# Performance work log

Measured on AMD Instinct MI355X. Metric: run time of the kernel, lower is better.

Reference implementation:

```python
import jax, jax.numpy as jnp
import numpy as np

H = 512        # hidden_dim
D_IN = 512     # input_dim
N_ACT = 16     # output_dim
DICT = 8192    # dict_len (episodic memory slots)
B = 4096       # batch
N_CYCLES = 10  # LCA iterations
DT_T = 0.6     # LCA dt/tau
EPS = 1e-8     # cosine-similarity eps


def setup_inputs() -> dict:
    key = jax.random.key(0)
    ks = jax.random.split(key, 12)
    NHT = 4 * H + 3  # (N_VSIG+1)*H + N_SSIG
    s = lambda i, shape, sc=1.0: jax.random.normal(ks[i], shape, jnp.float32) * sc
    return {
        "x_t": s(0, (1, B, D_IN)),
        "h_prev": s(1, (1, B, H), 0.1),
        "c_prev": s(2, (1, B, H), 0.1),
        "W_i2h": s(3, (NHT, D_IN), 1.0 / np.sqrt(D_IN)),
        "b_i2h": jnp.zeros((NHT,), jnp.float32),
        "W_h2h": s(4, (NHT, H), 1.0 / np.sqrt(H)),
        "b_h2h": jnp.zeros((NHT,), jnp.float32),
        "vals": s(5, (DICT, H), 0.1),  # episodic memory table
        "W_ih": s(6, (H, H), 1.0 / np.sqrt(H)),
        "b_ih": jnp.zeros((H,), jnp.float32),
        "W_actor": s(7, (N_ACT, H), 1.0 / np.sqrt(H)),
        "b_actor": jnp.zeros((N_ACT,), jnp.float32),
        "W_critic": s(8, (1, H), 1.0 / np.sqrt(H)),
        "b_critic": jnp.zeros((1,), jnp.float32),
        "mem_ptr": 0,
    }


def _lca(sim, leak, comp, w_input):
    # Leaky competing accumulator over memory slots; sim:[B,DICT], scalars:[B,1]
    ff = w_input * sim
    def step(V, _):
        inhib = comp * (jnp.sum(V, axis=-1, keepdims=True) - V)  # lateral inhibition (excl. self)
        V = jax.nn.relu(V + DT_T * (ff - leak * V - inhib))
        return V, None
    V, _ = jax.lax.scan(step, jnp.zeros_like(sim), None, length=N_CYCLES)
    return V


def reference(x_t, h_prev, c_prev, W_i2h, b_i2h, W_h2h, b_h2h, vals,
              W_ih, b_ih, W_actor, b_actor, W_critic, b_critic, mem_ptr):
    x, h, c = x_t[0], h_prev[0], c_prev[0]  # [B, dim]
    preact = x @ W_i2h.T + b_i2h + h @ W_h2h.T + b_h2h  # [B, 4H+3]
    gates = jax.nn.sigmoid(preact[:, :3 * H])
    f_t = gates[:, :H]
    o_t = gates[:, H:2 * H]
    i_t = gates[:, 2 * H:3 * H]
    inps = jax.nn.sigmoid(preact[:, 3 * H + 0])[:, None]  # input strength (gain=1)
    leak = jax.nn.sigmoid(preact[:, 3 * H + 1])[:, None]
    comp = jax.nn.sigmoid(preact[:, 3 * H + 2])[:, None]
    c_new = jnp.tanh(preact[:, 3 * H + 3:])
    c_t = c * f_t + i_t * c_new
    # --- recall: cosine similarity vs memory, then LCA competition ---
    qn = jnp.linalg.norm(c_t, axis=-1, keepdims=True)        # [B,1]
    mn = jnp.linalg.norm(vals, axis=-1, keepdims=True)       # [DICT,1]
    sim = (c_t @ vals.T) / jnp.maximum(qn * mn.T, EPS)       # [B,DICT]
    w = _lca(sim, leak, comp, inps)                          # [B,DICT]
    m_t = w @ vals                                           # [B,H]
    cm_t = c_t + m_t
    # --- encode: ring-buffer scatter write of cm_t into memory ---
    idx = (mem_ptr + jnp.arange(B)) % DICT
    new_vals = vals.at[idx].set(cm_t)
    h_t = o_t * jnp.tanh(cm_t)
    # --- A2C head ---
    a2c_h = jax.nn.relu(h_t @ W_ih.T + b_ih)
    pi = jax.nn.softmax(a2c_h @ W_actor.T + b_actor, axis=-1)
    value = a2c_h @ W_critic.T + b_critic
    return pi, value, h_t, cm_t, m_t, new_vals
```

## Files before the change

### kernel.cpp

```cpp
#include <hip/hip_runtime.h>
#include <hip/hip_fp16.h>
#include <math.h>

#define HH    512
#define DICT  8192
#define BATCH 4096
#define NCYC  10
#define DTT   0.6f

#define BM  128
#define BKT 64

using f16x8 = __attribute__((ext_vector_type(8))) _Float16;
using f32x4 = __attribute__((ext_vector_type(4))) float;

__device__ __forceinline__ float sigmoidf_(float x) { return 1.0f / (1.0f + __expf(-x)); }

__device__ __forceinline__ float waveReduceSum(float v) {
#pragma unroll
  for (int o = 1; o < 64; o <<= 1) v += __shfl_xor(v, o);
  return v;
}

__device__ __forceinline__ void gld16(const void* g, void* l) {
  __builtin_amdgcn_global_load_lds(
      (const __attribute__((address_space(1))) void*)g,
      (__attribute__((address_space(3))) void*)l, 16, 0, 0);
}

template<int ROWS>
__device__ __forceinline__ void stage_tile(const __half* gbase, int ld, char* lds, int tid) {
  constexpr int ISS = ROWS * 8 / 256;
#pragma unroll
  for (int i = 0; i < ISS; ++i) {
    int cidx = i * 256 + tid;
    int row  = cidx >> 3;
    int slot = cidx & 7;
    int k4   = slot ^ (row & 7);
    gld16(gbase + (size_t)row * ld + k4 * 8, lds + cidx * 16);
  }
}

__device__ __forceinline__ f16x8 frag_ld(const char* lds, int row, int kchunk) {
  int slot = kchunk ^ (row & 7);
  return *(const f16x8*)(lds + row * 128 + slot * 16);
}

template<int FN>
__device__ __forceinline__ void tile_mfma(const char* As, const char* Bs,
                                          int lane, int wr, int wc, f32x4 (&acc)[4][FN]) {
  const int g = lane >> 4, r = lane & 15;
#pragma unroll
  for (int ks = 0; ks < 2; ++ks) {
    f16x8 af[4], bfr[FN];
#pragma unroll
    for (int i = 0; i < 4; ++i)
      af[i] = frag_ld(As, wr * 64 + i * 16 + r, ks * 4 + g);
#pragma unroll
    for (int j = 0; j < FN; ++j)
      bfr[j] = frag_ld(Bs, wc * (FN * 16) + j * 16 + r, ks * 4 + g);
#pragma unroll
    for (int i = 0; i < 4; ++i)
#pragma unroll
      for (int j = 0; j < FN; ++j)
        acc[i][j] = __builtin_amdgcn_mfma_f32_16x16x32_f16(af[i], bfr[j], acc[i][j], 0, 0, 0);
  }
}

template<int BN, int FN>
__device__ __forceinline__ void gemm_seg(const __half* A, int lda, const __half* B, int ldb,
                                         int m0, int n0, int K, char* lds, int tid,
                                         f32x4 (&acc)[4][FN]) {
  constexpr int ABYTES = BM * BKT * 2;
  constexpr int BBYTES = BN * BKT * 2;
  const int lane = tid & 63, wid = tid >> 6;
  const int wr = wid >> 1, wc = wid & 1;
  const int nt = K / BKT;
  const __half* Ab = A + (size_t)m0 * lda;
  const __half* Bb = B + (size_t)n0 * ldb;
  stage_tile<BM>(Ab, lda, lds, tid);
  stage_tile<BN>(Bb, ldb, lds + ABYTES, tid);
  __syncthreads();
  int cur = 0;
  for (int t = 0; t < nt - 1; ++t) {
    char* nxt = lds + (cur ^ 1) * (ABYTES + BBYTES);
    stage_tile<BM>(Ab + (t + 1) * BKT, lda, nxt, tid);
    stage_tile<BN>(Bb + (t + 1) * BKT, ldb, nxt + ABYTES, tid);
    char* curb = lds + cur * (ABYTES + BBYTES);
    tile_mfma<FN>(curb, curb + ABYTES, lane, wr, wc, acc);
    __syncthreads();
    cur ^= 1;
  }
  char* curb = lds + cur * (ABYTES + BBYTES);
  tile_mfma<FN>(curb, curb + ABYTES, lane, wr, wc, acc);
  __syncthreads();
}

__device__ __forceinline__ void zero_acc4(f32x4 (&a)[4][4]) {
  f32x4 z = {0.f, 0.f, 0.f, 0.f};
#pragma unroll
  for (int i = 0; i < 4; ++i)
#pragma unroll
    for (int j = 0; j < 4; ++j) a[i][j] = z;
}
__device__ __forceinline__ void zero_acc2(f32x4 (&a)[4][2]) {
  f32x4 z = {0.f, 0.f, 0.f, 0.f};
#pragma unroll
  for (int i = 0; i < 4; ++i)
#pragma unroll
    for (int j = 0; j < 2; ++j) a[i][j] = z;
}

__global__ __launch_bounds__(256) void k_prep_cvt(
    const float* __restrict__ x, const float* __restrict__ h,
    const float* __restrict__ Wi, const float* __restrict__ Wh, const float* __restrict__ Wih,
    __half* __restrict__ x_h, __half* __restrict__ h_h,
    __half* __restrict__ Wip_h, __half* __restrict__ Whp_h, __half* __restrict__ Wih_h) {
  int gq = blockIdx.x * 256 + threadIdx.x;
  const float* src; __half* dst; int si, di;
  if (gq < 524288) {
    src = x; dst = x_h; si = di = gq * 4;
  } else if (gq < 1048576) {
    src = h; dst = h_h; si = di = (gq - 524288) * 4;
  } else if (gq < 1310720) {
    int iq = gq - 1048576;
    int jp = iq >> 7, k4 = (iq & 127) << 2;
    int U = jp >> 6, g = (jp >> 4) & 3, r = jp & 15;
    int u = U * 16 + r;
    int orig = g * 512 + u + (g == 3 ? 3 : 0);
    src = Wi; dst = Wip_h; si = orig * 512 + k4; di = jp * 512 + k4;
  } else if (gq < 1572864) {
    int iq = gq - 1310720;
    int jp = iq >> 7, k4 = (iq & 127) << 2;
    int U = jp >> 6, g = (jp >> 4) & 3, r = jp & 15;
    int u = U * 16 + r;
    int orig = g * 512 + u + (g == 3 ? 3 : 0);
    src = Wh; dst = Whp_h; si = orig * 512 + k4; di = jp * 512 + k4;
  } else if (gq < 1638400) {
    int iq = gq - 1572864;
    src = Wih; dst = Wih_h; si = di = iq * 4;
  } else return;
  float4 v = *(const float4*)(src + si);
  *(__half2*)(dst + di)     = __floats2half2_rn(v.x, v.y);
  *(__half2*)(dst + di + 2) = __floats2half2_rn(v.z, v.w);
}

__global__ __launch_bounds__(256) void k_prep_vals(
    const float* __restrict__ vals, float* __restrict__ nv,
    __half* __restrict__ vals_h, float* __restrict__ rmn) {
  const int row  = blockIdx.x * 4 + (threadIdx.x >> 6);
  const int lane = threadIdx.x & 63;
  const float* vr = vals + (size_t)row * HH + lane * 8;
  float4 a = *(const float4*)(vr);
  float4 b = *(const float4*)(vr + 4);
  float* nvp = nv + (size_t)row * HH + lane * 8;
  *(float4*)(nvp)     = a;
  *(float4*)(nvp + 4) = b;
  __half* vh = vals_h + (size_t)row * HH + lane * 8;
  *(__half2*)(vh)     = __floats2half2_rn(a.x, a.y);
  *(__half2*)(vh + 2) = __floats2half2_rn(a.z, a.w);
  *(__half2*)(vh + 4) = __floats2half2_rn(b.x, b.y);
  *(__half2*)(vh + 6) = __floats2half2_rn(b.z, b.w);
  float ss = a.x * a.x + a.y * a.y + a.z * a.z + a.w * a.w
           + b.x * b.x + b.y * b.y + b.z * b.z + b.w * b.w;
  ss = waveReduceSum(ss);
  if (lane == 0) rmn[row] = 1.f / fmaxf(sqrtf(ss), 1e-12f);
}

__global__ __launch_bounds__(256) void k_tr(const float* __restrict__ vals, __half* __restrict__ vT) {
  __shared__ float tile[32][33];
  int r0 = blockIdx.x * 32, c0 = blockIdx.y * 32;
  int tr = threadIdx.x >> 5, tc = threadIdx.x & 31;
#pragma unroll
  for (int p = 0; p < 4; ++p)
    tile[tr + p * 8][tc] = vals[(size_t)(r0 + tr + p * 8) * HH + c0 + tc];
  __syncthreads();
#pragma unroll
  for (int p = 0; p < 4; ++p)
    vT[(size_t)(c0 + tr + p * 8) * DICT + r0 + tc] = __float2half(tile[tc][tr + p * 8]);
}

__global__ __launch_bounds__(256) void k_preact(
    const __half* __restrict__ x_h, const __half* __restrict__ h_h,
    const __half* __restrict__ Wip, const __half* __restrict__ Whp,
    const float* __restrict__ bi, const float* __restrict__ bh,
    const float* __restrict__ c_prev,
    float* __restrict__ ct, float* __restrict__ ot, __half* __restrict__ ct_h) {
  __shared__ char smem[2 * (BM * BKT * 2 + 128 * BKT * 2)] __attribute__((aligned(16)));
  const int tid = threadIdx.x;
  const int m0 = blockIdx.y * 128, n0 = blockIdx.x * 128;
  f32x4 acc[4][4]; zero_acc4(acc);
  gemm_seg<128, 4>(x_h, HH, Wip, HH, m0, n0, HH, smem, tid, acc);
  gemm_seg<128, 4>(h_h, HH, Whp, HH, m0, n0, HH, smem, tid, acc);
  const int lane = tid & 63, wid = tid >> 6, wr = wid >> 1, wc = wid & 1;
  const int r = lane & 15;
  const int u = ((n0 >> 6) + wc) * 16 + r;
  float bsum[4];
#pragma unroll
  for (int g = 0; g < 4; ++g) {
    int orig = g * 512 + u + (g == 3 ? 3 : 0);
    bsum[g] = bi[orig] + bh[orig];
  }
#pragma unroll
  for (int fi = 0; fi < 4; ++fi)
#pragma unroll
    for (int q = 0; q < 4; ++q) {
      int m = m0 + wr * 64 + fi * 16 + (lane >> 4) * 4 + q;
      float f  = sigmoidf_(acc[fi][0][q] + bsum[0]);
      float o  = sigmoidf_(acc[fi][1][q] + bsum[1]);
      float ii = sigmoidf_(acc[fi][2][q] + bsum[2]);
      float cn = tanhf(acc[fi][3][q] + bsum[3]);
      size_t off = (size_t)m * HH + u;
      float cc = c_prev[off] * f + ii * cn;
      ct[off] = cc; ot[off] = o; ct_h[off] = __float2half(cc);
    }
}

__global__ __launch_bounds__(256) void k_scalars(
    const float* __restrict__ x, const float* __restrict__ h,
    const float* __restrict__ Wi, const float* __restrict__ Wh,
    const float* __restrict__ bi, const float* __restrict__ bh,
    const float* __restrict__ ct,
    float* __restrict__ inps, float* __restrict__ leak,
    float* __restrict__ comp, float* __restrict__ rqn) {
  const int b = blockIdx.x, wid = threadIdx.x >> 6, lane = threadIdx.x & 63;
  const int j = lane * 8;
  if (wid < 3) {
    const float* wi = Wi + (size_t)(1536 + wid) * HH + j;
    const float* wh = Wh + (size_t)(1536 + wid) * HH + j;
    const float* xr = x + (size_t)b * HH + j;
    const float* hr = h + (size_t)b * HH + j;
    float4 xa = *(const float4*)(xr), xb = *(const float4*)(xr + 4);
    float4 wa = *(const float4*)(wi), wb = *(const float4*)(wi + 4);
    float4 ha = *(const float4*)(hr), hb = *(const float4*)(hr + 4);
    float4 va = *(const float4*)(wh), vb = *(const float4*)(wh + 4);
    float s = xa.x * wa.x + xa.y * wa.y + xa.z * wa.z + xa.w * wa.w
            + xb.x * wb.x + xb.y * wb.y + xb.z * wb.z + xb.w * wb.w
            + ha.x * va.x + ha.y * va.y + ha.z * va.z + ha.w * va.w
            + hb.x * vb.x + hb.y * vb.y + hb.z * vb.z + hb.w * vb.w;
    s = waveReduceSum(s);
    if (lane == 0) {
      float v = sigmoidf_(s + bi[1536 + wid] + bh[1536 + wid]);
      if (wid == 0) inps[b] = v; else if (wid == 1) leak[b] = v; else comp[b] = v;
    }
  } else {
    const float* cr = ct + (size_t)b * HH + j;
    float4 a = *(const float4*)(cr), d = *(const float4*)(cr + 4);
    float ss = a.x * a.x + a.y * a.y + a.z * a.z + a.w * a.w
             + d.x * d.x + d.y * d.y + d.z * d.z + d.w * d.w;
    ss = waveReduceSum(ss);
    if (lane == 0) rqn[b] = 1.f / fmaxf(sqrtf(ss), 1e-12f);
  }
}

__global__ __launch_bounds__(256) void k_sim(
    const __half* __restrict__ ct_h, const __half* __restrict__ vals_h,
    const float* __restrict__ rqn, const float* __restrict__ rmn,
    __half* __restrict__ sim_h) {
  __shared__ char smem[2 * (BM * BKT * 2 + 128 * BKT * 2)] __attribute__((aligned(16)));
  const int tid = threadIdx.x;
  const int m0 = blockIdx.y * 128, n0 = blockIdx.x * 128;
  f32x4 acc[4][4]; zero_acc4(acc);
  gemm_seg<128, 4>(ct_h, HH, vals_h, HH, m0, n0, HH, smem, tid, acc);
  const int lane = tid & 63, wid = tid >> 6, wr = wid >> 1, wc = wid & 1;
#pragma unroll
  for (int fi = 0; fi < 4; ++fi)
#pragma unroll
    for (int fj = 0; fj < 4; ++fj)
#pragma unroll
      for (int q = 0; q < 4; ++q) {
        int m = m0 + wr * 64 + fi * 16 + (lane >> 4) * 4 + q;
        int n = n0 + wc * 64 + fj * 16 + (lane & 15);
        sim_h[(size_t)m * DICT + n] = __float2half(acc[fi][fj][q] * rqn[m] * rmn[n]);
      }
}

__global__ __launch_bounds__(256) void k_lca(
    const __half* __restrict__ sim_h, const float* __restrict__ inps,
    const float* __restrict__ leak, const float* __restrict__ comp,
    __half* __restrict__ w_h) {
  const int b = blockIdx.x, t = threadIdx.x;
  const __half* srow = sim_h + (size_t)b * DICT + t * 32;
  const float ffs = DTT * inps[b];
  const float a   = 1.0f - DTT * leak[b] + DTT * comp[b];
  const float cdt = DTT * comp[b];
  float ff[32], V[32];
#pragma unroll
  for (int i = 0; i < 4; ++i) {
    f16x8 v8 = *(const f16x8*)(srow + i * 8);
#pragma unroll
    for (int j = 0; j < 8; ++j) { ff[i * 8 + j] = ffs * (float)v8[j]; V[i * 8 + j] = 0.f; }
  }
  __shared__ float ps[4];
  for (int it = 0; it < NCYC; ++it) {
    float s = 0.f;
#pragma unroll
    for (int i = 0; i < 32; ++i) s += V[i];
    s = waveReduceSum(s);
    if ((t & 63) == 0) ps[t >> 6] = s;
    __syncthreads();
    float S = ps[0] + ps[1] + ps[2] + ps[3];
    __syncthreads();
    float sub = cdt * S;
#pragma unroll
    for (int i = 0; i < 32; ++i) V[i] = fmaxf(fmaf(a, V[i], ff[i] - sub), 0.f);
  }
  __half* wrow = w_h + (size_t)b * DICT + t * 32;
#pragma unroll
  for (int i = 0; i < 4; ++i) {
    f16x8 o8;
#pragma unroll
    for (int j = 0; j < 8; ++j) o8[j] = (_Float16)V[i * 8 + j];
    *(f16x8*)(wrow + i * 8) = o8;
  }
}

__global__ __launch_bounds__(256) void k_mt_p(
    const __half* __restrict__ w_h, const __half* __restrict__ vT_h,
    float* __restrict__ partial) {
  __shared__ char smem[2 * (BM * BKT * 2 + 64 * BKT * 2)] __attribute__((aligned(16)));
  const int tid = threadIdx.x, bid = blockIdx.x;
  const int xcd = bid & 7, idx = bid >> 3;
  const int n = idx & 7, q = idx >> 3;
  const int g = (q << 3) | xcd;
  const int m = g >> 2, s = g & 3;
  const int m0 = m * 128, n0 = n * 64;
  f32x4 acc[4][2]; zero_acc2(acc);
  gemm_seg<64, 2>(w_h + s * 2048, DICT, vT_h + s * 2048, DICT, m0, n0, 2048, smem, tid, acc);
  const int lane = tid & 63, wid = tid >> 6, wr = wid >> 1, wc = wid & 1;
  float* pbase = partial + (size_t)s * (BATCH * HH);
#pragma unroll
  for (int fi = 0; fi < 4; ++fi)
#pragma unroll
    for (int fj = 0; fj < 2; ++fj)
#pragma unroll
      for (int qq = 0; qq < 4; ++qq) {
        int mm = m0 + wr * 64 + fi * 16 + (lane >> 4) * 4 + qq;
        int nn = n0 + wc * 32 + fj * 16 + (lane & 15);
        pbase[(size_t)mm * HH + nn] = acc[fi][fj][qq];
      }
}

__global__ __launch_bounds__(256) void k_mt_red(
    const float* __restrict__ partial,
    const float* __restrict__ ct, const float* __restrict__ ot, const int* __restrict__ mptr,
    float* __restrict__ out_mt, float* __restrict__ out_cmt, float* __restrict__ out_ht,
    float* __restrict__ out_nv, __half* __restrict__ ht_h) {
  const int i4 = blockIdx.x * 256 + threadIdx.x;
  const size_t off = (size_t)i4 * 4;
  const int m = i4 >> 7;
  float4 p  = *(const float4*)(partial + off);
  float4 p1 = *(const float4*)(partial + 2097152 + off);
  float4 p2 = *(const float4*)(partial + 4194304 + off);
  float4 p3 = *(const float4*)(partial + 6291456 + off);
  p.x += p1.x + p2.x + p3.x;
  p.y += p1.y + p2.y + p3.y;
  p.z += p1.z + p2.z + p3.z;
  p.w += p1.w + p2.w + p3.w;
  float4 c4 = *(const float4*)(ct + off);
  float4 o4 = *(const float4*)(ot + off);
  float4 cm, hv;
  cm.x = c4.x + p.x; hv.x = o4.x * tanhf(cm.x);
  cm.y = c4.y + p.y; hv.y = o4.y * tanhf(cm.y);
  cm.z = c4.z + p.z; hv.z = o4.z * tanhf(cm.z);
  cm.w = c4.w + p.w; hv.w = o4.w * tanhf(cm.w);
  *(float4*)(out_mt + off)  = p;
  *(float4*)(out_cmt + off) = cm;
  *(float4*)(out_ht + off)  = hv;
  *(__half2*)(ht_h + off)     = __floats2half2_rn(hv.x, hv.y);
  *(__half2*)(ht_h + off + 2) = __floats2half2_rn(hv.z, hv.w);
  const int nvrow = (mptr[0] + m) & (DICT - 1);
  *(float4*)(out_nv + (size_t)nvrow * HH + (off & 511)) = cm;
}

__global__ __launch_bounds__(256) void k_a2c(
    const __half* __restrict__ ht_h, const __half* __restrict__ Wih_h,
    const float* __restrict__ bih, float* __restrict__ a2c) {
  __shared__ char smem[2 * (BM * BKT * 2 + 64 * BKT * 2)] __attribute__((aligned(16)));
  const int tid = threadIdx.x;
  const int bid = blockIdx.x;
  const int xn = (bid >> 3) & 7, ym = (bid & 7) | ((bid >> 6) << 3);
  const int m0 = ym * 128, n0 = xn * 64;
  f32x4 acc[4][2]; zero_acc2(acc);
  gemm_seg<64, 2>(ht_h, HH, Wih_h, HH, m0, n0, HH, smem, tid, acc);
  const int lane = tid & 63, wid = tid >> 6, wr = wid >> 1, wc = wid & 1;
#pragma unroll
  for (int fi = 0; fi < 4; ++fi)
#pragma unroll
    for (int fj = 0; fj < 2; ++fj)
#pragma unroll
      for (int q = 0; q < 4; ++q) {
        int m = m0 + wr * 64 + fi * 16 + (lane >> 4) * 4 + q;
        int n = n0 + wc * 32 + fj * 16 + (lane & 15);
        a2c[(size_t)m * HH + n] = fmaxf(acc[fi][fj][q] + bih[n], 0.f);
      }
}

__global__ __launch_bounds__(256) void k_actor(
    const float* __restrict__ a2c,
    const float* __restrict__ Wact, const float* __restrict__ bact,
    const float* __restrict__ Wcr, const float* __restrict__ bcr,
    float* __restrict__ out_pi, float* __restrict__ out_val) {
  const int b = blockIdx.x * 4 + (threadIdx.x >> 6);
  const int lane = threadIdx.x & 63;
  const float* hrow = a2c + (size_t)b * HH;
  float4 a0 = *(const float4*)(hrow + (lane << 3));
  float4 a1 = *(const float4*)(hrow + (lane << 3) + 4);
  float lg[17];
#pragma unroll
  for (int o = 0; o < 17; ++o) {
    const float* wr = (o < 16) ? (Wact + (size_t)o * HH) : Wcr;
    float4 w0 = *(const float4*)(wr + (lane << 3));
    float4 w1 = *(const float4*)(wr + (lane << 3) + 4);
    float s = a0.x * w0.x + a0.y * w0.y + a0.z * w0.z + a0.w * w0.w
            + a1.x * w1.x + a1.y * w1.y + a1.z * w1.z + a1.w * w1.w;
    lg[o] = waveReduceSum(s);
  }
#pragma unroll
  for (int o = 0; o < 16; ++o) lg[o] += bact[o];
  float mx = lg[0];
#pragma unroll
  for (int o = 1; o < 16; ++o) mx = fmaxf(mx, lg[o]);
  float e[16], sum = 0.f;
#pragma unroll
  for (int o = 0; o < 16; ++o) { e[o] = __expf(lg[o] - mx); sum += e[o]; }
  float rs = 1.f / sum;
  if (lane == 0) {
#pragma unroll
    for (int o = 0; o < 16; ++o) out_pi[(size_t)b * 16 + o] = e[o] * rs;
    out_val[b] = lg[16] + bcr[0];
  }
}

extern "C" void kernel_launch(void* const* d_in, const int* in_sizes, int n_in,
                              void* d_out, int out_size, void* d_ws, size_t ws_size,
                              hipStream_t stream) {
  const float* x    = (const float*)d_in[0];
  const float* h    = (const float*)d_in[1];
  const float* c    = (const float*)d_in[2];
  const float* Wi   = (const float*)d_in[3];
  const float* bi   = (const float*)d_in[4];
  const float* Wh   = (const float*)d_in[5];
  const float* bh   = (const float*)d_in[6];
  const float* vals = (const float*)d_in[7];
  const float* Wih  = (const float*)d_in[8];
  const float* bih  = (const float*)d_in[9];
  const float* Wact = (const float*)d_in[10];
  const float* bact = (const float*)d_in[11];
  const float* Wcr  = (const float*)d_in[12];
  const float* bcr  = (const float*)d_in[13];
  const int*   mptr = (const int*)d_in[14];

  float* F = (float*)d_ws;
  __half* w_h    = (__half*)F;
  __half* sim_h   = (__half*)(F + 16777216);
  float*  a2c     = F + 16777216;
  float*  partial = F + 33554432;
  float*  ct     = F + 50331648;
  float*  ot     = F + 52428800;
  __half* ct_h   = (__half*)(F + 54525952);
  __half* vals_h = (__half*)(F + 55574528);
  __half* vT_h   = (__half*)(F + 57671680);
  __half* x_h    = (__half*)(F + 59768832);
  __half* ht_h   = x_h;
  __half* h_h    = (__half*)(F + 60817408);
  __half* Wip_h  = (__half*)(F + 61865984);
  __half* Whp_h  = (__half*)(F + 62423040);
  __half* Wih_h  = (__half*)(F + 62980096);
  float*  inps   = F + 63111168;
  float*  leak   = inps + 4096;
  float*  comp   = leak + 4096;
  float*  rqn    = comp + 4096;
  float*  rmn    = rqn + 4096;

  float* out     = (float*)d_out;
  float* out_pi  = out;
  float* out_val = out + 65536;
  float* out_ht  = out + 69632;
  float* out_cmt = out_ht + 2097152;
  float* out_mt  = out_cmt + 2097152;
  float* out_nv  = out_mt + 2097152;

  dim3 b256(256);
  k_prep_cvt <<<6400, b256, 0, stream>>>(x, h, Wi, Wh, Wih, x_h, h_h, Wip_h, Whp_h, Wih_h);
  k_prep_vals<<<2048, b256, 0, stream>>>(vals, out_nv, vals_h, rmn);
  k_tr <<<dim3(256, 16), b256, 0, stream>>>(vals, vT_h);
  k_preact <<<dim3(16, 32), b256, 0, stream>>>(x_h, h_h, Wip_h, Whp_h, bi, bh, c,
                                               ct, ot, ct_h);
  k_scalars<<<BATCH, b256, 0, stream>>>(x, h, Wi, Wh, bi, bh, ct, inps, leak, comp, rqn);
  k_sim    <<<dim3(64, 32), b256, 0, stream>>>(ct_h, vals_h, rqn, rmn, sim_h);
  k_lca    <<<BATCH, b256, 0, stream>>>(sim_h, inps, leak, comp, w_h);
  k_mt_p   <<<1024, b256, 0, stream>>>(w_h, vT_h, partial);
  k_mt_red <<<2048, b256, 0, stream>>>(partial, ct, ot, mptr,
                                       out_mt, out_cmt, out_ht, out_nv, ht_h);
  k_a2c    <<<256, b256, 0, stream>>>(ht_h, Wih_h, bih, a2c);
  k_actor  <<<BATCH / 4, b256, 0, stream>>>(a2c, Wact, bact, Wcr, bcr, out_pi, out_val);
}
```

Measured before the change: 234.8 us.

## Single-buffer GEMM LDS staging and merge three prep kernels into one launch

The shared GEMM segment drops its LDS double buffering. Each K-tile is now staged, synced, computed and synced again, which halves shared memory per block and may allow more resident blocks. The three prep kernels (fp16 conversion, vals copy/norm, vals transpose) are merged into one launch dispatched by block index, removing two launches. The cost is that global loads no longer overlap MFMA work inside each block, and each K-tile gets an extra barrier.

```diff
diff --git a/kernel.cpp b/kernel.cpp
--- a/kernel.cpp
+++ b/kernel.cpp
@@ -72,28 +72,18 @@
                                          int m0, int n0, int K, char* lds, int tid,
                                          f32x4 (&acc)[4][FN]) {
   constexpr int ABYTES = BM * BKT * 2;
-  constexpr int BBYTES = BN * BKT * 2;
   const int lane = tid & 63, wid = tid >> 6;
   const int wr = wid >> 1, wc = wid & 1;
   const int nt = K / BKT;
   const __half* Ab = A + (size_t)m0 * lda;
   const __half* Bb = B + (size_t)n0 * ldb;
-  stage_tile<BM>(Ab, lda, lds, tid);
-  stage_tile<BN>(Bb, ldb, lds + ABYTES, tid);
-  __syncthreads();
-  int cur = 0;
-  for (int t = 0; t < nt - 1; ++t) {
-    char* nxt = lds + (cur ^ 1) * (ABYTES + BBYTES);
-    stage_tile<BM>(Ab + (t + 1) * BKT, lda, nxt, tid);
-    stage_tile<BN>(Bb + (t + 1) * BKT, ldb, nxt + ABYTES, tid);
-    char* curb = lds + cur * (ABYTES + BBYTES);
-    tile_mfma<FN>(curb, curb + ABYTES, lane, wr, wc, acc);
+  for (int t = 0; t < nt; ++t) {
+    stage_tile<BM>(Ab + t * BKT, lda, lds, tid);
+    stage_tile<BN>(Bb + t * BKT, ldb, lds + ABYTES, tid);
     __syncthreads();
-    cur ^= 1;
-  }
-  char* curb = lds + cur * (ABYTES + BBYTES);
-  tile_mfma<FN>(curb, curb + ABYTES, lane, wr, wc, acc);
-  __syncthreads();
+    tile_mfma<FN>(lds, lds + ABYTES, lane, wr, wc, acc);
+    __syncthreads();
+  }
 }
 
 __device__ __forceinline__ void zero_acc4(f32x4 (&a)[4][4]) {
@@ -111,73 +101,74 @@
     for (int j = 0; j < 2; ++j) a[i][j] = z;
 }
 
-__global__ __launch_bounds__(256) void k_prep_cvt(
+__global__ __launch_bounds__(256) void k_prep(
     const float* __restrict__ x, const float* __restrict__ h,
     const float* __restrict__ Wi, const float* __restrict__ Wh, const float* __restrict__ Wih,
+    const float* __restrict__ vals,
     __half* __restrict__ x_h, __half* __restrict__ h_h,
-    __half* __restrict__ Wip_h, __half* __restrict__ Whp_h, __half* __restrict__ Wih_h) {
-  int gq = blockIdx.x * 256 + threadIdx.x;
-  const float* src; __half* dst; int si, di;
-  if (gq < 524288) {
-    src = x; dst = x_h; si = di = gq * 4;
-  } else if (gq < 1048576) {
-    src = h; dst = h_h; si = di = (gq - 524288) * 4;
-  } else if (gq < 1310720) {
-    int iq = gq - 1048576;
-    int jp = iq >> 7, k4 = (iq & 127) << 2;
-    int U = jp >> 6, g = (jp >> 4) & 3, r = jp & 15;
-    int u = U * 16 + r;
-    int orig = g * 512 + u + (g == 3 ? 3 : 0);
-    src = Wi; dst = Wip_h; si = orig * 512 + k4; di = jp * 512 + k4;
-  } else if (gq < 1572864) {
-    int iq = gq - 1310720;
-    int jp = iq >> 7, k4 = (iq & 127) << 2;
-    int U = jp >> 6, g = (jp >> 4) & 3, r = jp & 15;
-    int u = U * 16 + r;
-    int orig = g * 512 + u + (g == 3 ? 3 : 0);
-    src = Wh; dst = Whp_h; si = orig * 512 + k4; di = jp * 512 + k4;
-  } else if (gq < 1638400) {
-    int iq = gq - 1572864;
-    src = Wih; dst = Wih_h; si = di = iq * 4;
-  } else return;
-  float4 v = *(const float4*)(src + si);
-  *(__half2*)(dst + di)     = __floats2half2_rn(v.x, v.y);
-  *(__half2*)(dst + di + 2) = __floats2half2_rn(v.z, v.w);
-}
-
-__global__ __launch_bounds__(256) void k_prep_vals(
-    const float* __restrict__ vals, float* __restrict__ nv,
-    __half* __restrict__ vals_h, float* __restrict__ rmn) {
-  const int row  = blockIdx.x * 4 + (threadIdx.x >> 6);
-  const int lane = threadIdx.x & 63;
-  const float* vr = vals + (size_t)row * HH + lane * 8;
-  float4 a = *(const float4*)(vr);
-  float4 b = *(const float4*)(vr + 4);
-  float* nvp = nv + (size_t)row * HH + lane * 8;
-  *(float4*)(nvp)     = a;
-  *(float4*)(nvp + 4) = b;
-  __half* vh = vals_h + (size_t)row * HH + lane * 8;
-  *(__half2*)(vh)     = __floats2half2_rn(a.x, a.y);
-  *(__half2*)(vh + 2) = __floats2half2_rn(a.z, a.w);
-  *(__half2*)(vh + 4) = __floats2half2_rn(b.x, b.y);
-  *(__half2*)(vh + 6) = __floats2half2_rn(b.z, b.w);
-  float ss = a.x * a.x + a.y * a.y + a.z * a.z + a.w * a.w
-           + b.x * b.x + b.y * b.y + b.z * b.z + b.w * b.w;
-  ss = waveReduceSum(ss);
-  if (lane == 0) rmn[row] = 1.f / fmaxf(sqrtf(ss), 1e-12f);
-}
-
-__global__ __launch_bounds__(256) void k_tr(const float* __restrict__ vals, __half* __restrict__ vT) {
+    __half* __restrict__ Wip_h, __half* __restrict__ Whp_h, __half* __restrict__ Wih_h,
+    float* __restrict__ nv, __half* __restrict__ vals_h, float* __restrict__ rmn,
+    __half* __restrict__ vT) {
   __shared__ float tile[32][33];
-  int r0 = blockIdx.x * 32, c0 = blockIdx.y * 32;
-  int tr = threadIdx.x >> 5, tc = threadIdx.x & 31;
-#pragma unroll
-  for (int p = 0; p < 4; ++p)
-    tile[tr + p * 8][tc] = vals[(size_t)(r0 + tr + p * 8) * HH + c0 + tc];
-  __syncthreads();
-#pragma unroll
-  for (int p = 0; p < 4; ++p)
-    vT[(size_t)(c0 + tr + p * 8) * DICT + r0 + tc] = __float2half(tile[tc][tr + p * 8]);
+  const int bid = blockIdx.x;
+  if (bid < 6400) {
+    int gq = bid * 256 + threadIdx.x;
+    const float* src; __half* dst; int si, di;
+    if (gq < 524288) {
+      src = x; dst = x_h; si = di = gq * 4;
+    } else if (gq < 1048576) {
+      src = h; dst = h_h; si = di = (gq - 524288) * 4;
+    } else if (gq < 1310720) {
+      int iq = gq - 1048576;
+      int jp = iq >> 7, k4 = (iq & 127) << 2;
+      int U = jp >> 6, g = (jp >> 4) & 3, r = jp & 15;
+      int u = U * 16 + r;
+      int orig = g * 512 + u + (g == 3 ? 3 : 0);
+      src = Wi; dst = Wip_h; si = orig * 512 + k4; di = jp * 512 + k4;
+    } else if (gq < 1572864) {
+      int iq = gq - 1310720;
+      int jp = iq >> 7, k4 = (iq & 127) << 2;
+      int U = jp >> 6, g = (jp >> 4) & 3, r = jp & 15;
+      int u = U * 16 + r;
+      int orig = g * 512 + u + (g == 3 ? 3 : 0);
+      src = Wh; dst = Whp_h; si = orig * 512 + k4; di = jp * 512 + k4;
+    } else if (gq < 1638400) {
+      int iq = gq - 1572864;
+      src = Wih; dst = Wih_h; si = di = iq * 4;
+    } else return;
+    float4 v = *(const float4*)(src + si);
+    *(__half2*)(dst + di)     = __floats2half2_rn(v.x, v.y);
+    *(__half2*)(dst + di + 2) = __floats2half2_rn(v.z, v.w);
+  } else if (bid < 8448) {
+    const int row  = (bid - 6400) * 4 + (threadIdx.x >> 6);
+    const int lane = threadIdx.x & 63;
+    const float* vr = vals + (size_t)row * HH + lane * 8;
+    float4 a = *(const float4*)(vr);
+    float4 b = *(const float4*)(vr + 4);
+    float* nvp = nv + (size_t)row * HH + lane * 8;
+    *(float4*)(nvp)     = a;
+    *(float4*)(nvp + 4) = b;
+    __half* vh = vals_h + (size_t)row * HH + lane * 8;
+    *(__half2*)(vh)     = __floats2half2_rn(a.x, a.y);
+    *(__half2*)(vh + 2) = __floats2half2_rn(a.z, a.w);
+    *(__half2*)(vh + 4) = __floats2half2_rn(b.x, b.y);
+    *(__half2*)(vh + 6) = __floats2half2_rn(b.z, b.w);
+    float ss = a.x * a.x + a.y * a.y + a.z * a.z + a.w * a.w
+             + b.x * b.x + b.y * b.y + b.z * b.z + b.w * b.w;
+    ss = waveReduceSum(ss);
+    if (lane == 0) rmn[row] = 1.f / fmaxf(sqrtf(ss), 1e-12f);
+  } else {
+    const int idx = bid - 8448;
+    const int r0 = (idx & 255) * 32, c0 = (idx >> 8) * 32;
+    const int tr = threadIdx.x >> 5, tc = threadIdx.x & 31;
+#pragma unroll
+    for (int p = 0; p < 4; ++p)
+      tile[tr + p * 8][tc] = vals[(size_t)(r0 + tr + p * 8) * HH + c0 + tc];
+    __syncthreads();
+#pragma unroll
+    for (int p = 0; p < 4; ++p)
+      vT[(size_t)(c0 + tr + p * 8) * DICT + r0 + tc] = __float2half(tile[tc][tr + p * 8]);
+  }
 }
 
 __global__ __launch_bounds__(256) void k_preact(
@@ -186,7 +177,7 @@
     const float* __restrict__ bi, const float* __restrict__ bh,
     const float* __restrict__ c_prev,
     float* __restrict__ ct, float* __restrict__ ot, __half* __restrict__ ct_h) {
-  __shared__ char smem[2 * (BM * BKT * 2 + 128 * BKT * 2)] __attribute__((aligned(16)));
+  __shared__ char smem[BM * BKT * 2 + 128 * BKT * 2] __attribute__((aligned(16)));
   const int tid = threadIdx.x;
   const int m0 = blockIdx.y * 128, n0 = blockIdx.x * 128;
   f32x4 acc[4][4]; zero_acc4(acc);
@@ -257,7 +248,7 @@
     const __half* __restrict__ ct_h, const __half* __restrict__ vals_h,
     const float* __restrict__ rqn, const float* __restrict__ rmn,
     __half* __restrict__ sim_h) {
-  __shared__ char smem[2 * (BM * BKT * 2 + 128 * BKT * 2)] __attribute__((aligned(16)));
+  __shared__ char smem[BM * BKT * 2 + 128 * BKT * 2] __attribute__((aligned(16)));
   const int tid = threadIdx.x;
   const int m0 = blockIdx.y * 128, n0 = blockIdx.x * 128;
   f32x4 acc[4][4]; zero_acc4(acc);
@@ -318,7 +309,7 @@
 __global__ __launch_bounds__(256) void k_mt_p(
     const __half* __restrict__ w_h, const __half* __restrict__ vT_h,
     float* __restrict__ partial) {
-  __shared__ char smem[2 * (BM * BKT * 2 + 64 * BKT * 2)] __attribute__((aligned(16)));
+  __shared__ char smem[BM * BKT * 2 + 64 * BKT * 2] __attribute__((aligned(16)));
   const int tid = threadIdx.x, bid = blockIdx.x;
   const int xcd = bid & 7, idx = bid >> 3;
   const int n = idx & 7, q = idx >> 3;
@@ -376,7 +367,7 @@
 __global__ __launch_bounds__(256) void k_a2c(
     const __half* __restrict__ ht_h, const __half* __restrict__ Wih_h,
     const float* __restrict__ bih, float* __restrict__ a2c) {
-  __shared__ char smem[2 * (BM * BKT * 2 + 64 * BKT * 2)] __attribute__((aligned(16)));
+  __shared__ char smem[BM * BKT * 2 + 64 * BKT * 2] __attribute__((aligned(16)));
   const int tid = threadIdx.x;
   const int bid = blockIdx.x;
   const int xn = (bid >> 3) & 7, ym = (bid & 7) | ((bid >> 6) << 3);
@@ -482,9 +473,9 @@
   float* out_nv  = out_mt + 2097152;
 
   dim3 b256(256);
-  k_prep_cvt <<<6400, b256, 0, stream>>>(x, h, Wi, Wh, Wih, x_h, h_h, Wip_h, Whp_h, Wih_h);
-  k_prep_vals<<<2048, b256, 0, stream>>>(vals, out_nv, vals_h, rmn);
-  k_tr <<<dim3(256, 16), b256, 0, stream>>>(vals, vT_h);
+  k_prep   <<<12544, b256, 0, stream>>>(x, h, Wi, Wh, Wih, vals,
+                                        x_h, h_h, Wip_h, Whp_h, Wih_h,
+                                        out_nv, vals_h, rmn, vT_h);
   k_preact <<<dim3(16, 32), b256, 0, stream>>>(x_h, h_h, Wip_h, Whp_h, bi, bh, c,
                                                ct, ot, ct_h);
   k_scalars<<<BATCH, b256, 0, stream>>>(x, h, Wi, Wh, bi, bh, ct, inps, leak, comp, rqn);
```

After: 221.6 us. 5.6% less time.
